# Kernel optimization log

Hardware: AMD Instinct MI355X
Metric: run time of the kernel (lower is better)

Reference implementation:

```python
import jax, jax.numpy as jnp
import numpy as np

B, T, F = 8, 1024, 64
DM, L = 256, 4            # d_model, n_layers
DI, N, DC = 2 * DM, 16, 4  # d_inner, d_state, d_conv
DTR = DM // 16             # dt_rank = ceil(256/16) = 16


def setup_inputs() -> dict:
    key = jax.random.key(0)
    ks = jax.random.split(key, 16)
    rn = lambda k, shp, fan: jax.random.normal(k, shp, jnp.float32) / np.sqrt(fan)
    inp = {
        "x": jax.random.normal(ks[0], (B, T, F), jnp.float32),
        "proj_w": rn(ks[1], (DM, F), F),
        "proj_b": jnp.zeros((DM,), jnp.float32),
        "in_proj_w": rn(ks[2], (L, 2 * DI, DM), DM),
        "conv_w": rn(ks[3], (L, DI, DC), DC),
        "conv_b": jnp.zeros((L, DI), jnp.float32),
        "x_proj_w": rn(ks[4], (L, DTR + 2 * N, DI), DI),
        "dt_proj_w": rn(ks[5], (L, DI, DTR), DTR),
        "dt_proj_b": jax.random.normal(ks[6], (L, DI), jnp.float32) * 0.1 - 4.0,
        "A_log": jnp.log(jnp.broadcast_to(jnp.arange(1, N + 1, dtype=jnp.float32), (L, DI, N))),
        "Dp": jnp.ones((L, DI), jnp.float32),
        "out_proj_w": rn(ks[7], (L, DM, DI), DI),
        "ln_g": jnp.ones((DM,), jnp.float32),
        "ln_b": jnp.zeros((DM,), jnp.float32),
        "head_w": rn(ks[8], (1, DM), DM),
        "head_b": jnp.zeros((1,), jnp.float32),
    }
    return inp


def mamba_layer(x, ipw, cw, cb, xpw, dtw, dtb, Alog, Dvec, opw):
    # x: [B, T, DM]
    Bn, Tn, _ = x.shape
    xz = jnp.einsum('btd,ed->bte', x, ipw)        # [B,T,2*DI]
    xc, z = jnp.split(xz, 2, axis=-1)             # each [B,T,DI]
    # causal depthwise conv1d, kernel DC, pad left DC-1
    xp = jnp.pad(xc, ((0, 0), (DC - 1, 0), (0, 0)))
    xc = sum(xp[:, k:k + Tn, :] * cw[:, k] for k in range(DC)) + cb
    xc = jax.nn.silu(xc)
    xdbl = jnp.einsum('btd,ed->bte', xc, xpw)     # [B,T,DTR+2N]
    dt = jax.nn.softplus(jnp.einsum('btr,dr->btd', xdbl[..., :DTR], dtw) + dtb)
    Bm = xdbl[..., DTR:DTR + N]                   # [B,T,N]
    Cm = xdbl[..., DTR + N:]                      # [B,T,N]
    A = -jnp.exp(Alog)                            # [DI,N]

    def step(h, inp):
        dt_t, B_t, C_t, u_t = inp                 # [B,DI],[B,N],[B,N],[B,DI]
        dA = jnp.exp(dt_t[:, :, None] * A)        # [B,DI,N]
        h = dA * h + (dt_t * u_t)[:, :, None] * B_t[:, None, :]
        y = jnp.einsum('bdn,bn->bd', h, C_t)
        return h, y

    h0 = jnp.zeros((Bn, DI, N), x.dtype)
    inps = (dt.transpose(1, 0, 2), Bm.transpose(1, 0, 2),
            Cm.transpose(1, 0, 2), xc.transpose(1, 0, 2))
    _, ys = jax.lax.scan(step, h0, inps)          # ys: [T,B,DI]
    y = ys.transpose(1, 0, 2) + Dvec * xc
    y = y * jax.nn.silu(z)
    return jnp.einsum('btd,ed->bte', y, opw)      # [B,T,DM]


def reference(x, proj_w, proj_b, in_proj_w, conv_w, conv_b, x_proj_w,
              dt_proj_w, dt_proj_b, A_log, Dp, out_proj_w,
              ln_g, ln_b, head_w, head_b):
    h = jnp.einsum('btf,df->btd', x, proj_w) + proj_b
    for i in range(L):
        h = mamba_layer(h, in_proj_w[i], conv_w[i], conv_b[i], x_proj_w[i],
                        dt_proj_w[i], dt_proj_b[i], A_log[i], Dp[i], out_proj_w[i])
    mu = h.mean(-1, keepdims=True)
    var = ((h - mu) ** 2).mean(-1, keepdims=True)
    hn = (h - mu) * jax.lax.rsqrt(var + 1e-5) * ln_g + ln_b
    last = hn[:, -1, :]                            # [B,DM]
    logits = last @ head_w.T + head_b              # [B,1]
    return logits.squeeze(-1)
```

## Files before the change

### kernel.cpp

```cpp
#include <hip/hip_runtime.h>
#include <math.h>

#define TT 1024
#define DII 512
#define DMM 256
#define NC 32
#define TC 32

typedef double dx4 __attribute__((ext_vector_type(4)));
typedef float fx4 __attribute__((ext_vector_type(4)));

template <int BM>
__global__ __launch_bounds__(256) void gemm_mfma(
    const float* __restrict__ A, const float* __restrict__ W,
    float* __restrict__ C0, float* __restrict__ C1,
    int split, int ldc0, int ldc1, const float* __restrict__ bias,
    int K)
{
  const int RT = BM / 32;
  const int LDA = BM + 1;
  const int NF4 = BM / 64;
  __shared__ double As[16 * (BM + 1)];
  __shared__ double Bs[16 * 65];
  int tid = threadIdx.x;
  int row0 = blockIdx.y * BM;
  int e0 = blockIdx.x * 64;
  int wave = tid >> 6, lid = tid & 63;
  int wy = wave >> 1, wx = wave & 1;
  int i16 = lid & 15, k4 = lid >> 4;

  dx4 acc[RT][2];
#pragma unroll
  for (int rt = 0; rt < RT; ++rt) {
    acc[rt][0] = dx4{0., 0., 0., 0.};
    acc[rt][1] = dx4{0., 0., 0., 0.};
  }

  fx4 pA[NF4], pB;
#pragma unroll
  for (int i = 0; i < NF4; ++i) {
    int l4 = (tid + 256 * i) * 4;
    pA[i] = *(const fx4*)(A + (size_t)(row0 + (l4 >> 4)) * K + (l4 & 15));
  }
  {
    int l4 = tid * 4;
    pB = *(const fx4*)(W + (size_t)(e0 + (l4 >> 4)) * K + (l4 & 15));
  }

  for (int k0 = 0;; k0 += 16) {
#pragma unroll
    for (int i = 0; i < NF4; ++i) {
      int l4 = (tid + 256 * i) * 4;
      int m = l4 >> 4, kk = l4 & 15;
#pragma unroll
      for (int j = 0; j < 4; ++j)
        As[(kk + j) * LDA + m] = (double)pA[i][j];
    }
    {
      int l4 = tid * 4;
      int m = l4 >> 4, kk = l4 & 15;
#pragma unroll
      for (int j = 0; j < 4; ++j)
        Bs[(kk + j) * 65 + m] = (double)pB[j];
    }
    __syncthreads();
    bool more = (k0 + 16 < K);
    if (more) {
      int kn = k0 + 16;
#pragma unroll
      for (int i = 0; i < NF4; ++i) {
        int l4 = (tid + 256 * i) * 4;
        pA[i] = *(const fx4*)(A + (size_t)(row0 + (l4 >> 4)) * K + kn + (l4 & 15));
      }
      {
        int l4 = tid * 4;
        pB = *(const fx4*)(W + (size_t)(e0 + (l4 >> 4)) * K + kn + (l4 & 15));
      }
    }
#pragma unroll
    for (int kk0 = 0; kk0 < 16; kk0 += 4) {
      int krow = (kk0 + k4) * LDA + wy * (RT * 16);
      int krowB = (kk0 + k4) * 65 + wx * 32;
      double b0 = Bs[krowB + i16];
      double b1 = Bs[krowB + 16 + i16];
#pragma unroll
      for (int rt = 0; rt < RT; ++rt) {
        double a = As[krow + rt * 16 + i16];
        acc[rt][0] = __builtin_amdgcn_mfma_f64_16x16x4f64(a, b0, acc[rt][0], 0, 0, 0);
        acc[rt][1] = __builtin_amdgcn_mfma_f64_16x16x4f64(a, b1, acc[rt][1], 0, 0, 0);
      }
    }
    __syncthreads();
    if (!more) break;
  }

  int rowbase = row0 + wy * (RT * 16) + k4 * 4;
  int colb = e0 + wx * 32;
#pragma unroll
  for (int rt = 0; rt < RT; ++rt)
#pragma unroll
    for (int ct = 0; ct < 2; ++ct) {
      int e = colb + ct * 16 + i16;
      double bv = bias ? (double)bias[e] : 0.0;
#pragma unroll
      for (int r = 0; r < 4; ++r) {
        int row = rowbase + rt * 16 + r;
        float v = (float)(acc[rt][ct][r] + bv);
        if (e < split) C0[(size_t)row * ldc0 + e] = v;
        else           C1[(size_t)row * ldc1 + (e - split)] = v;
      }
    }
}

__global__ __launch_bounds__(256) void gemm_small(
    const float* __restrict__ A, const float* __restrict__ W,
    double* __restrict__ C, int K)
{
  __shared__ float As[16][33];
  __shared__ float Bs[16][49];
  int tx = threadIdx.x, ty = threadIdx.y;
  int tid = ty * 16 + tx;
  int row0 = blockIdx.x * 32;
  double acc[2][3] = {{0., 0., 0.}, {0., 0., 0.}};
  for (int k0 = 0; k0 < K; k0 += 16) {
    for (int l = tid; l < 32 * 16; l += 256) {
      int m = l >> 4, kk = l & 15;
      As[kk][m] = A[(size_t)(row0 + m) * K + k0 + kk];
    }
    for (int l = tid; l < 48 * 16; l += 256) {
      int e = l >> 4, kk = l & 15;
      Bs[kk][e] = W[(size_t)e * K + k0 + kk];
    }
    __syncthreads();
#pragma unroll
    for (int kk = 0; kk < 16; ++kk) {
      double a0 = (double)As[kk][ty], a1 = (double)As[kk][16 + ty];
      double b0 = (double)Bs[kk][tx], b1 = (double)Bs[kk][16 + tx], b2 = (double)Bs[kk][32 + tx];
      acc[0][0] = fma(a0, b0, acc[0][0]);
      acc[0][1] = fma(a0, b1, acc[0][1]);
      acc[0][2] = fma(a0, b2, acc[0][2]);
      acc[1][0] = fma(a1, b0, acc[1][0]);
      acc[1][1] = fma(a1, b1, acc[1][1]);
      acc[1][2] = fma(a1, b2, acc[1][2]);
    }
    __syncthreads();
  }
#pragma unroll
  for (int i = 0; i < 2; ++i)
#pragma unroll
    for (int j = 0; j < 3; ++j)
      C[(size_t)(row0 + ty + 16 * i) * 48 + (tx + 16 * j)] = acc[i][j];
}

__global__ __launch_bounds__(256) void conv_silu_k(
    const float* __restrict__ xzx, const float* __restrict__ cw,
    const float* __restrict__ cb, float* __restrict__ uf)
{
  int idx = blockIdx.x * 256 + threadIdx.x;
  int dv = (idx & 127) * 4;
  int row = idx >> 7;
  int t = row & (TT - 1);
  fx4 cwv[4];
#pragma unroll
  for (int i = 0; i < 4; ++i) cwv[i] = *(const fx4*)(cw + (dv + i) * 4);
  fx4 cbv = *(const fx4*)(cb + dv);
  double acc[4];
#pragma unroll
  for (int i = 0; i < 4; ++i) acc[i] = (double)cbv[i];
#pragma unroll
  for (int k = 0; k < 4; ++k) {
    int ts = t + k - 3;
    if (ts >= 0) {
      fx4 xv = *(const fx4*)(xzx + (size_t)(row + k - 3) * DII + dv);
#pragma unroll
      for (int i = 0; i < 4; ++i)
        acc[i] = fma((double)xv[i], (double)cwv[i][k], acc[i]);
    }
  }
  fx4 outv;
#pragma unroll
  for (int i = 0; i < 4; ++i) {
    double s = 1.0 / (1.0 + exp(-acc[i]));
    outv[i] = (float)(acc[i] * s);
  }
  *(fx4*)(uf + (size_t)row * DII + dv) = outv;
}

__global__ __launch_bounds__(256) void dt_gate_k(
    const double* __restrict__ xdbl, const float* __restrict__ dtw,
    const float* __restrict__ dtb, float* __restrict__ dtf,
    float* __restrict__ rbf, float* __restrict__ zb)
{
  int idx = blockIdx.x * 256 + threadIdx.x;
  int d = idx & (DII - 1);
  int row = idx >> 9;
  double s = 0.0;
#pragma unroll
  for (int j = 0; j < 16; ++j)
    s = fma(xdbl[(size_t)row * 48 + j], (double)dtw[d * 16 + j], s);
  s += (double)dtb[d];
  double e = exp(s);
  double dtv = (s > 30.0) ? s : log1p(e);
  dtf[idx] = (float)dtv;
  rbf[idx] = (float)(1.0 / (1.0 + e));
  double zz = (double)zb[idx];
  zb[idx] = (float)(zz / (1.0 + exp(-zz)));
}

__global__ __launch_bounds__(256) void en_k(
    const float* __restrict__ Alog, double* __restrict__ enb)
{
  int idx = blockIdx.x * 256 + threadIdx.x;
  int n = idx & 15;
  enb[idx] = (double)(n + 1) - exp((double)Alog[idx]);
}

__global__ __launch_bounds__(256) void scan_pass1(
    const float* __restrict__ dtp, const float* __restrict__ rbf,
    const float* __restrict__ u, const double* __restrict__ xdbl,
    const double* __restrict__ enb,
    double* __restrict__ Pout, double* __restrict__ Hout)
{
  __shared__ double Bsh[TC * 16];
  int bc = blockIdx.x >> 2;
  size_t base48 = (size_t)bc * TC * 48;
  for (int idx = threadIdx.x; idx < TC * 16; idx += 256) {
    int t = idx >> 4, j = idx & 15;
    Bsh[idx] = xdbl[base48 + t * 48 + 16 + j];
  }
  __syncthreads();

  int tid = blockIdx.x * 256 + threadIdx.x;
  int half = tid & 1;
  int d = (tid >> 1) & (DII - 1);
  int c = (tid >> 10) & (NC - 1);
  int b = tid >> 15;
  int n0 = half * 8;
  double en[8];
  {
    const dx4* ep = (const dx4*)(enb + d * 16 + n0);
    dx4 e0 = ep[0], e1 = ep[1];
    en[0] = e0[0]; en[1] = e0[1]; en[2] = e0[2]; en[3] = e0[3];
    en[4] = e1[0]; en[5] = e1[1]; en[6] = e1[2]; en[7] = e1[3];
  }
  size_t o = ((size_t)b * TT + c * TC) * DII + d;
  double h[8], P[8];
#pragma unroll
  for (int j = 0; j < 8; ++j) { h[j] = 0.0; P[j] = 1.0; }
  float rv = rbf[o], dtv = dtp[o], uu = u[o];
  for (int t = 0; t < TC; ++t) {
    float rn = 0.f, dtn = 0.f, un = 0.f;
    if (t < TC - 1) {
      size_t o2 = o + DII;
      rn = rbf[o2]; dtn = dtp[o2]; un = u[o2];
    }
    double r = (double)rv;
    double dtd = (double)dtv;
    double dtu = dtd * (double)uu;
    dx4 B0 = ((const dx4*)(Bsh + t * 16 + n0))[0];
    dx4 B1 = ((const dx4*)(Bsh + t * 16 + n0))[1];
    double Bj[8] = {B0[0], B0[1], B0[2], B0[3], B1[0], B1[1], B1[2], B1[3]};
    double r2 = r * r, r4 = r2 * r2;
    double p = half ? (r4 * r4 * r) : r;
#pragma unroll
    for (int j = 0; j < 8; ++j) {
      double dA = p * fma(dtd, en[j], 1.0);
      p *= r;
      h[j] = fma(dA, h[j], dtu * Bj[j]);
      P[j] *= dA;
    }
    o += DII;
    rv = rn; dtv = dtn; uu = un;
  }
  dx4* Pp = (dx4*)(Pout + (size_t)tid * 8);
  dx4* Hp = (dx4*)(Hout + (size_t)tid * 8);
  Pp[0] = dx4{P[0], P[1], P[2], P[3]};
  Pp[1] = dx4{P[4], P[5], P[6], P[7]};
  Hp[0] = dx4{h[0], h[1], h[2], h[3]};
  Hp[1] = dx4{h[4], h[5], h[6], h[7]};
}

__global__ __launch_bounds__(256) void scan_pass2(
    double* __restrict__ P, const double* __restrict__ Hend)
{
  int tid = blockIdx.x * 256 + threadIdx.x;
  int n = tid & 15;
  int d = (tid >> 4) & (DII - 1);
  int b = tid >> 13;
  double h = 0.0;
#pragma unroll
  for (int c = 0; c < NC; ++c) {
    size_t o = (((size_t)((b * NC + c) * DII + d)) << 4) + n;
    double Pv = P[o];
    P[o] = h;
    h = fma(Pv, h, Hend[o]);
  }
}

__global__ __launch_bounds__(256) void scan_pass3(
    float* __restrict__ yout, const float* __restrict__ dtp,
    const float* __restrict__ rbf, const float* __restrict__ u,
    const double* __restrict__ xdbl,
    const double* __restrict__ enb, const double* __restrict__ hin,
    const float* __restrict__ gz, const float* __restrict__ Dp)
{
  __shared__ double Bsh[TC * 32];
  int bc = blockIdx.x >> 2;
  size_t base48 = (size_t)bc * TC * 48;
  for (int idx = threadIdx.x; idx < TC * 32; idx += 256) {
    int t = idx >> 5, j = idx & 31;
    Bsh[idx] = xdbl[base48 + t * 48 + 16 + j];
  }
  __syncthreads();

  int tid = blockIdx.x * 256 + threadIdx.x;
  int half = tid & 1;
  int d = (tid >> 1) & (DII - 1);
  int c = (tid >> 10) & (NC - 1);
  int b = tid >> 15;
  int n0 = half * 8;
  double en[8];
  {
    const dx4* ep = (const dx4*)(enb + d * 16 + n0);
    dx4 e0 = ep[0], e1 = ep[1];
    en[0] = e0[0]; en[1] = e0[1]; en[2] = e0[2]; en[3] = e0[3];
    en[4] = e1[0]; en[5] = e1[1]; en[6] = e1[2]; en[7] = e1[3];
  }
  double Dpd = (double)Dp[d];
  size_t o = ((size_t)b * TT + c * TC) * DII + d;
  double h[8];
  {
    const dx4* hp = (const dx4*)(hin + (size_t)tid * 8);
    dx4 h0 = hp[0], h1 = hp[1];
    h[0] = h0[0]; h[1] = h0[1]; h[2] = h0[2]; h[3] = h0[3];
    h[4] = h1[0]; h[5] = h1[1]; h[6] = h1[2]; h[7] = h1[3];
  }
  float rv = rbf[o], dtv = dtp[o], uu = u[o], gzv = gz[o];
  for (int t = 0; t < TC; ++t) {
    float rn = 0.f, dtn = 0.f, un = 0.f, gzn = 0.f;
    if (t < TC - 1) {
      size_t o2 = o + DII;
      rn = rbf[o2]; dtn = dtp[o2]; un = u[o2]; gzn = gz[o2];
    }
    double r = (double)rv;
    double dtd = (double)dtv;
    double uud = (double)uu;
    double dtu = dtd * uud;
    dx4 B0 = ((const dx4*)(Bsh + t * 32 + n0))[0];
    dx4 B1 = ((const dx4*)(Bsh + t * 32 + n0))[1];
    dx4 C0 = ((const dx4*)(Bsh + t * 32 + 16 + n0))[0];
    dx4 C1 = ((const dx4*)(Bsh + t * 32 + 16 + n0))[1];
    double Bj[8] = {B0[0], B0[1], B0[2], B0[3], B1[0], B1[1], B1[2], B1[3]};
    double Cj[8] = {C0[0], C0[1], C0[2], C0[3], C1[0], C1[1], C1[2], C1[3]};
    double r2 = r * r, r4 = r2 * r2;
    double p = half ? (r4 * r4 * r) : r;
    double y = 0.0;
#pragma unroll
    for (int j = 0; j < 8; ++j) {
      double dA = p * fma(dtd, en[j], 1.0);
      p *= r;
      h[j] = fma(dA, h[j], dtu * Bj[j]);
      y = fma(h[j], Cj[j], y);
    }
    y += __shfl_xor(y, 1);
    if (!half) yout[o] = (float)(fma(Dpd, uud, y) * (double)gzv);
    o += DII;
    rv = rn; dtv = dtn; uu = un; gzv = gzn;
  }
}

__global__ __launch_bounds__(256) void ln_head_k(
    const float* __restrict__ hbuf, const float* __restrict__ g,
    const float* __restrict__ be, const float* __restrict__ hw,
    const float* __restrict__ hb, float* __restrict__ out)
{
  __shared__ double arr[256];
  __shared__ double mu, var;
  int b = blockIdx.x, d = threadIdx.x;
  double v = (double)hbuf[((size_t)b * TT + (TT - 1)) * DMM + d];
  arr[d] = v; __syncthreads();
  if (d == 0) { double s = 0; for (int i = 0; i < 256; ++i) s += arr[i]; mu = s / 256.0; }
  __syncthreads();
  double diff = v - mu;
  arr[d] = diff * diff; __syncthreads();
  if (d == 0) { double s = 0; for (int i = 0; i < 256; ++i) s += arr[i]; var = s / 256.0; }
  __syncthreads();
  double hn = diff * (1.0 / sqrt(var + 1e-5)) * (double)g[d] + (double)be[d];
  arr[d] = hn * (double)hw[d]; __syncthreads();
  if (d == 0) { double s = 0; for (int i = 0; i < 256; ++i) s += arr[i]; out[b] = (float)(s + (double)hb[0]); }
}

extern "C" void kernel_launch(void* const* d_in, const int* in_sizes, int n_in,
                              void* d_out, int out_size, void* d_ws, size_t ws_size,
                              hipStream_t stream)
{
  (void)in_sizes; (void)n_in; (void)out_size; (void)ws_size;
  const float* x    = (const float*)d_in[0];
  const float* pw   = (const float*)d_in[1];
  const float* pb   = (const float*)d_in[2];
  const float* ipw  = (const float*)d_in[3];
  const float* cw   = (const float*)d_in[4];
  const float* cb   = (const float*)d_in[5];
  const float* xpw  = (const float*)d_in[6];
  const float* dtw  = (const float*)d_in[7];
  const float* dtb  = (const float*)d_in[8];
  const float* alog = (const float*)d_in[9];
  const float* Dp   = (const float*)d_in[10];
  const float* opw  = (const float*)d_in[11];
  const float* lng  = (const float*)d_in[12];
  const float* lnb  = (const float*)d_in[13];
  const float* hw   = (const float*)d_in[14];
  const float* hb   = (const float*)d_in[15];
  float* out = (float*)d_out;

  float*  rbf  = (float*)d_ws;
  double* xdbl = (double*)(rbf + (size_t)8192 * 512);
  double* enb  = xdbl + (size_t)8192 * 48;
  float*  hbuf = (float*)(enb + 32768);
  float*  xzx  = hbuf + (size_t)8192 * 256;
  float*  zb   = xzx + (size_t)8192 * 512;
  float*  yb   = zb + (size_t)8192 * 512;
  float*  uf   = yb + (size_t)8192 * 512;
  float*  dtf  = uf + (size_t)8192 * 512;
  double* Pbuf = (double*)xzx;
  double* Hend = (double*)yb;

  en_k<<<128, 256, 0, stream>>>(alog, enb);

  gemm_mfma<64><<<dim3(4, 128), 256, 0, stream>>>(x, pw, hbuf, nullptr, 256, 256, 256, pb, 64);

  for (int i = 0; i < 4; ++i) {
    gemm_mfma<128><<<dim3(16, 64), 256, 0, stream>>>(hbuf, ipw + (size_t)i * 1024 * 256,
                                                     xzx, zb, 512, 512, 512, nullptr, 256);
    conv_silu_k<<<4096, 256, 0, stream>>>(xzx, cw + i * 2048, cb + i * 512, uf);
    gemm_small<<<256, dim3(16, 16), 0, stream>>>(uf, xpw + (size_t)i * 48 * 512, xdbl, 512);
    dt_gate_k<<<16384, 256, 0, stream>>>(xdbl, dtw + i * 8192, dtb + i * 512, dtf, rbf, zb);
    scan_pass1<<<1024, 256, 0, stream>>>(dtf, rbf, uf, xdbl, enb + i * 8192, Pbuf, Hend);
    scan_pass2<<<256, 256, 0, stream>>>(Pbuf, Hend);
    scan_pass3<<<1024, 256, 0, stream>>>(yb, dtf, rbf, uf, xdbl, enb + i * 8192, Pbuf,
                                         zb, Dp + i * 512);
    gemm_mfma<64><<<dim3(4, 128), 256, 0, stream>>>(yb, opw + (size_t)i * 256 * 512,
                                                    hbuf, nullptr, 256, 256, 256, nullptr, 512);
  }
  ln_head_k<<<8, 256, 0, stream>>>(hbuf, lng, lnb, hw, hb, out);
}
```

Measured before the change: 1.298 ms.

## Double-buffer GEMM tiles with direct global-to-LDS loads and swizzled float layout

Replaces the register-staged, double-converted shared-memory tiles in the FP64-MFMA GEMM with float tiles filled by global_load_lds into two LDS buffers, synchronized by manual vmcnt waits and barriers. It uses an XOR swizzle on the k-groups to avoid bank conflicts and converts to double at read time. The goal is to overlap global loads with MFMA compute and halve LDS footprint and store traffic. Risks include the hand-written waitcnt counts being wrong, and the loop assumes NT is even.

```diff
diff --git a/kernel.cpp b/kernel.cpp
--- a/kernel.cpp
+++ b/kernel.cpp
@@ -17,17 +17,26 @@
     int split, int ldc0, int ldc1, const float* __restrict__ bias,
     int K)
 {
-  const int RT = BM / 32;
-  const int LDA = BM + 1;
-  const int NF4 = BM / 64;
-  __shared__ double As[16 * (BM + 1)];
-  __shared__ double Bs[16 * 65];
-  int tid = threadIdx.x;
-  int row0 = blockIdx.y * BM;
-  int e0 = blockIdx.x * 64;
-  int wave = tid >> 6, lid = tid & 63;
-  int wy = wave >> 1, wx = wave & 1;
-  int i16 = lid & 15, k4 = lid >> 4;
+  constexpr int RT = BM / 32;
+  constexpr int NAI = BM / 64;
+  constexpr int LPT = NAI + 1;
+  __shared__ __align__(16) float As[2][BM * 16];
+  __shared__ __align__(16) float Bs[2][64 * 16];
+  const int tid = threadIdx.x;
+  const int wave = tid >> 6, lid = tid & 63;
+  const int wy = wave >> 1, wx = wave & 1;
+  const int i16 = lid & 15, k4 = lid >> 4;
+  const int row0 = blockIdx.y * BM, e0 = blockIdx.x * 64;
+
+  const int lr = lid >> 2;
+  const int kg = ((lid & 3) ^ ((lid >> 3) & 3)) << 2;
+  const int swz = (i16 >> 1) & 3;
+
+  const float* gA[NAI];
+#pragma unroll
+  for (int j = 0; j < NAI; ++j)
+    gA[j] = A + (size_t)(row0 + wave * (16 * NAI) + j * 16 + lr) * K + kg;
+  const float* gB = W + (size_t)(e0 + wave * 16 + lr) * K + kg;
 
   dx4 acc[RT][2];
 #pragma unroll
@@ -36,63 +45,66 @@
     acc[rt][1] = dx4{0., 0., 0., 0.};
   }
 
-  fx4 pA[NF4], pB;
-#pragma unroll
-  for (int i = 0; i < NF4; ++i) {
-    int l4 = (tid + 256 * i) * 4;
-    pA[i] = *(const fx4*)(A + (size_t)(row0 + (l4 >> 4)) * K + (l4 & 15));
-  }
-  {
-    int l4 = tid * 4;
-    pB = *(const fx4*)(W + (size_t)(e0 + (l4 >> 4)) * K + (l4 & 15));
-  }
-
-  for (int k0 = 0;; k0 += 16) {
-#pragma unroll
-    for (int i = 0; i < NF4; ++i) {
-      int l4 = (tid + 256 * i) * 4;
-      int m = l4 >> 4, kk = l4 & 15;
-#pragma unroll
-      for (int j = 0; j < 4; ++j)
-        As[(kk + j) * LDA + m] = (double)pA[i][j];
-    }
-    {
-      int l4 = tid * 4;
-      int m = l4 >> 4, kk = l4 & 15;
-#pragma unroll
-      for (int j = 0; j < 4; ++j)
-        Bs[(kk + j) * 65 + m] = (double)pB[j];
-    }
-    __syncthreads();
-    bool more = (k0 + 16 < K);
-    if (more) {
-      int kn = k0 + 16;
-#pragma unroll
-      for (int i = 0; i < NF4; ++i) {
-        int l4 = (tid + 256 * i) * 4;
-        pA[i] = *(const fx4*)(A + (size_t)(row0 + (l4 >> 4)) * K + kn + (l4 & 15));
-      }
-      {
-        int l4 = tid * 4;
-        pB = *(const fx4*)(W + (size_t)(e0 + (l4 >> 4)) * K + kn + (l4 & 15));
-      }
-    }
+  typedef __attribute__((address_space(1))) const void* gp_t;
+  typedef __attribute__((address_space(3))) void* lp_t;
+
+  auto issue = [&](int t, int b) {
+    const int k0 = t << 4;
+#pragma unroll
+    for (int j = 0; j < NAI; ++j)
+      __builtin_amdgcn_global_load_lds((gp_t)(gA[j] + k0),
+                                       (lp_t)&As[b][(wave * NAI + j) * 256],
+                                       16, 0, 0);
+    __builtin_amdgcn_global_load_lds((gp_t)(gB + k0),
+                                     (lp_t)&Bs[b][wave * 256], 16, 0, 0);
+  };
+
+  auto compute = [&](int b) {
 #pragma unroll
     for (int kk0 = 0; kk0 < 16; kk0 += 4) {
-      int krow = (kk0 + k4) * LDA + wy * (RT * 16);
-      int krowB = (kk0 + k4) * 65 + wx * 32;
-      double b0 = Bs[krowB + i16];
-      double b1 = Bs[krowB + 16 + i16];
+      const int kc = k4 + (((kk0 >> 2) ^ swz) << 2);
+      double b0 = (double)Bs[b][(wx * 32 + i16) * 16 + kc];
+      double b1 = (double)Bs[b][(wx * 32 + 16 + i16) * 16 + kc];
 #pragma unroll
       for (int rt = 0; rt < RT; ++rt) {
-        double a = As[krow + rt * 16 + i16];
+        double a = (double)As[b][(wy * (RT * 16) + rt * 16 + i16) * 16 + kc];
         acc[rt][0] = __builtin_amdgcn_mfma_f64_16x16x4f64(a, b0, acc[rt][0], 0, 0, 0);
         acc[rt][1] = __builtin_amdgcn_mfma_f64_16x16x4f64(a, b1, acc[rt][1], 0, 0, 0);
       }
     }
-    __syncthreads();
-    if (!more) break;
-  }
+  };
+
+#define GWAIT3() asm volatile("s_waitcnt vmcnt(3)" ::: "memory")
+#define GWAIT2() asm volatile("s_waitcnt vmcnt(2)" ::: "memory")
+#define GWAIT0() asm volatile("s_waitcnt vmcnt(0)" ::: "memory")
+#define GBAR()   asm volatile("s_barrier" ::: "memory")
+
+  const int NT = K >> 4;
+  issue(0, 0);
+  issue(1, 1);
+  for (int t = 0; t < NT; t += 2) {
+    if (LPT == 3) GWAIT3(); else GWAIT2();
+    GBAR();
+    compute(0);
+    GBAR();
+    if (t + 2 < NT) {
+      issue(t + 2, 0);
+      if (LPT == 3) GWAIT3(); else GWAIT2();
+      GBAR();
+      compute(1);
+      GBAR();
+      issue(t + 3, 1);
+    } else {
+      GWAIT0();
+      GBAR();
+      compute(1);
+      GBAR();
+    }
+  }
+#undef GWAIT3
+#undef GWAIT2
+#undef GWAIT0
+#undef GBAR
 
   int rowbase = row0 + wy * (RT * 16) + k4 * 4;
   int colb = e0 + wx * 32;
```

New measurement: 1.277 ms. About the same (-1.6%).
